# Performance work log

Hardware: AMD Instinct MI355X
Metric: run time of the kernel (lower is better)

Reference implementation:

```python
import jax, jax.numpy as jnp
import numpy as np

S, O, T, C, H = 32, 64, 91, 128, 8  # scenes, objects, timesteps, dim, heads


def setup_inputs() -> dict:
    key = jax.random.key(0)
    ks = jax.random.split(key, 6)
    x = jax.random.normal(ks[0], (S, O, T, C), dtype=jnp.float32)
    valid_mask = jax.random.randint(ks[1], (S, O, T), 0, 2) > 0

    def lin(k, shape):
        return jax.random.normal(k, shape, dtype=jnp.float32) / np.float32(np.sqrt(shape[-1]))

    return dict(
        x=x,
        valid_mask=valid_mask,
        Wqkv_a=lin(ks[2], (3 * C, C)), Wproj_a=lin(ks[3], (C, C)), bproj_a=jnp.zeros((C,), jnp.float32),
        Wqkv_t=lin(ks[4], (3 * C, C)), Wproj_t=lin(ks[5], (C, C)), bproj_t=jnp.zeros((C,), jnp.float32),
    )


def _masked_mha(x, mask, Wqkv, Wproj, bproj):
    # x: (B, N, C); mask: (B, N, N) bool. qkv has no bias, proj has bias.
    B, N, Cd = x.shape
    hd = Cd // H
    scale = hd ** (-0.5)
    qkv = (x @ Wqkv.T).reshape(B, N, 3, H, hd).transpose(2, 0, 3, 1, 4)
    q, k, v = qkv[0], qkv[1], qkv[2]  # (B, H, N, hd)
    s = jnp.einsum('bhnd,bhmd->bhnm', q, k) * scale
    s = jnp.where(mask[:, None], s, -jnp.inf)
    # rows that are fully masked are set to all-zeros (-> uniform softmax), as in torch code
    dead = jnp.all(~mask, axis=-1)  # (B, N)
    s = jnp.where(dead[:, None, :, None], jnp.float32(0.0), s)
    a = jax.nn.softmax(s, axis=-1)
    o = jnp.einsum('bhnm,bhmd->bhnd', a, v).transpose(0, 2, 1, 3).reshape(B, N, Cd)
    return o @ Wproj.T + bproj


def reference(x, valid_mask, Wqkv_a, Wproj_a, bproj_a, Wqkv_t, Wproj_t, bproj_t):
    S_, O_, T_, C_ = x.shape
    # agent-wise attention: attend across objects at each (scene, timestep)
    xa = x.transpose(0, 2, 1, 3).reshape(S_ * T_, O_, C_)
    ma = valid_mask.transpose(0, 2, 1)  # (S, T, O)
    ma = (ma[..., :, None] & ma[..., None, :]).reshape(S_ * T_, O_, O_)
    xa = _masked_mha(xa, ma, Wqkv_a, Wproj_a, bproj_a)
    # time-wise attention: attend across timesteps for each (scene, object)
    xt = xa.reshape(S_, T_, O_, C_).transpose(0, 2, 1, 3).reshape(S_ * O_, T_, C_)
    mt = (valid_mask[..., :, None] & valid_mask[..., None, :]).reshape(S_ * O_, T_, T_)
    xt = _masked_mha(xt, mt, Wqkv_t, Wproj_t, bproj_t)
    return xt.reshape(S_, O_, T_, C_)
```

## Files before the change

### kernel.cpp

```cpp
#include <hip/hip_runtime.h>

#define S_ 32
#define O_ 64
#define T_ 91
#define C_ 128
#define H_ 8

typedef __attribute__((ext_vector_type(8))) short short8;
typedef __attribute__((ext_vector_type(4))) short short4b;
typedef __attribute__((ext_vector_type(4))) float f32x4;

__device__ short g_wqa_h[384 * 128], g_wqa_l[384 * 128];
__device__ short g_wqt_h[384 * 128], g_wqt_l[384 * 128];
__device__ short g_wpa_h[128 * 128], g_wpa_l[128 * 128];
__device__ short g_wpt_h[128 * 128], g_wpt_l[128 * 128];

__device__ __forceinline__ void splitf(float f, short& h, short& l) {
    unsigned u = __float_as_uint(f);
    float hf = __uint_as_float(u & 0xffff0000u);
    h = (short)(u >> 16);
    l = (short)(__float_as_uint(f - hf) >> 16);
}

__device__ __forceinline__ void split8g(const float* p, short8& h, short8& l) {
    float4 a = *(const float4*)p;
    float4 b = *(const float4*)(p + 4);
    float v[8] = {a.x, a.y, a.z, a.w, b.x, b.y, b.z, b.w};
    #pragma unroll
    for (int j = 0; j < 8; ++j) { short hh, ll; splitf(v[j], hh, ll); h[j] = hh; l[j] = ll; }
}

__device__ __forceinline__ void split4v(f32x4 v, short4b& h, short4b& l) {
    #pragma unroll
    for (int j = 0; j < 4; ++j) { short hh, ll; splitf(v[j], hh, ll); h[j] = hh; l[j] = ll; }
}

__global__ __launch_bounds__(256) void prep_all(
    const float* __restrict__ wqa, const float* __restrict__ wqt,
    const float* __restrict__ wpa, const float* __restrict__ wpt)
{
    int t = blockIdx.x * 256 + threadIdx.x;
    const float* src; short* dh; short* dl; int idx;
    if (t < 6144)       { src = wqa; dh = g_wqa_h; dl = g_wqa_l; idx = t; }
    else if (t < 12288) { src = wqt; dh = g_wqt_h; dl = g_wqt_l; idx = t - 6144; }
    else if (t < 14336) { src = wpa; dh = g_wpa_h; dl = g_wpa_l; idx = t - 12288; }
    else                { src = wpt; dh = g_wpt_h; dl = g_wpt_l; idx = t - 14336; }
    int c = idx >> 4, gk = idx & 15;
    int kp = gk >> 2, gg = gk & 3;
    int ct = c >> 4, cl = c & 15;
    const float* s = src + (long)c * C_ + gk * 8;
    long slot = (long)ct * 2048 + kp * 512 + (cl + 16 * gg) * 8;
    short8 vh, vl;
    split8g(s, vh, vl);
    *(short8*)(dh + slot) = vh;
    *(short8*)(dl + slot) = vl;
}

template<int N, int NT, int PASS>
__global__ __launch_bounds__(512) void fused_pass(
    const float* __restrict__ xg, const int* __restrict__ mask,
    const float* __restrict__ bproj, float* __restrict__ yout,
    int bdiv, long bs1, long bs2, long ts, long m1, long m2)
{
    constexpr bool FULL = (NT * 16 == N);
    extern __shared__ char smem[];
    short* xh = (short*)smem;
    short* xl = xh + NT * 2048;
    short* yh = xh;
    short* yl = xl;
    int*   s_m = (int*)(smem + NT * 8192);

    const short* Wh = (PASS == 0) ? g_wqa_h : g_wqt_h;
    const short* Wl = (PASS == 0) ? g_wqa_l : g_wqt_l;
    const short* Ph = (PASS == 0) ? g_wpa_h : g_wpt_h;
    const short* Pl = (PASS == 0) ? g_wpa_l : g_wpt_l;

    const int tid = threadIdx.x;
    const int wv = tid >> 6, l = tid & 63;
    const int ic = l & 15, g = l >> 4;
    const int b = blockIdx.x;
    const int s = b / bdiv, u = b - s * bdiv;
    const long xbase = (long)s * bs1 + (long)u * bs2;
    const long mbase = (long)s * (O_ * T_) + (long)u * m1;

    for (int gi = tid; gi < NT * 256; gi += 512) {
        int token = gi >> 4, cg = gi & 15;
        int kp = cg >> 2, gg = cg & 3;
        int slot = ((token >> 4) * 4 + kp) * 512 + (gg * 16 + (token & 15)) * 8;
        short8 vh, vl;
        if (FULL || token < N) {
            split8g(xg + xbase + (long)token * ts + cg * 8, vh, vl);
        } else {
            #pragma unroll
            for (int j = 0; j < 8; ++j) { vh[j] = 0; vl[j] = 0; }
        }
        *(short8*)(xh + slot) = vh;
        *(short8*)(xl + slot) = vl;
    }
    for (int idx = tid; idx < NT * 16; idx += 512)
        s_m[idx] = (idx < N) ? (mask[mbase + (long)idx * m2] != 0) : 0;
    __syncthreads();

    unsigned jbits = 0, mbits = 0;
    #pragma unroll
    for (int jt = 0; jt < NT; ++jt)
        #pragma unroll
        for (int r = 0; r < 4; ++r) {
            int j = jt * 16 + 4 * g + r;
            if (j < N) {
                jbits |= 1u << (jt * 4 + r);
                if (s_m[j]) mbits |= 1u << (jt * 4 + r);
            }
        }

    const int h = wv;
    f32x4 aQ[NT], aK[NT], aV[NT];
    #pragma unroll
    for (int t2 = 0; t2 < NT; ++t2) {
        aQ[t2] = (f32x4){0.f,0.f,0.f,0.f};
        aK[t2] = (f32x4){0.f,0.f,0.f,0.f};
        aV[t2] = (f32x4){0.f,0.f,0.f,0.f};
    }
    #pragma unroll
    for (int kp = 0; kp < 4; ++kp) {
        short8 wqh = *(const short8*)(Wh + (h * 4 + kp) * 512 + l * 8);
        short8 wql = *(const short8*)(Wl + (h * 4 + kp) * 512 + l * 8);
        short8 wkh = *(const short8*)(Wh + ((8 + h) * 4 + kp) * 512 + l * 8);
        short8 wkl = *(const short8*)(Wl + ((8 + h) * 4 + kp) * 512 + l * 8);
        short8 wvh = *(const short8*)(Wh + ((16 + h) * 4 + kp) * 512 + l * 8);
        short8 wvl = *(const short8*)(Wl + ((16 + h) * 4 + kp) * 512 + l * 8);
        #pragma unroll
        for (int tt = 0; tt < NT; ++tt) {
            short8 xhv = *(const short8*)(xh + (tt * 4 + kp) * 512 + l * 8);
            short8 xlv = *(const short8*)(xl + (tt * 4 + kp) * 512 + l * 8);
            aQ[tt] = __builtin_amdgcn_mfma_f32_16x16x32_bf16(wqh, xhv, aQ[tt], 0, 0, 0);
            aQ[tt] = __builtin_amdgcn_mfma_f32_16x16x32_bf16(wql, xhv, aQ[tt], 0, 0, 0);
            aQ[tt] = __builtin_amdgcn_mfma_f32_16x16x32_bf16(wqh, xlv, aQ[tt], 0, 0, 0);
            aK[tt] = __builtin_amdgcn_mfma_f32_16x16x32_bf16(wkh, xhv, aK[tt], 0, 0, 0);
            aK[tt] = __builtin_amdgcn_mfma_f32_16x16x32_bf16(wkl, xhv, aK[tt], 0, 0, 0);
            aK[tt] = __builtin_amdgcn_mfma_f32_16x16x32_bf16(wkh, xlv, aK[tt], 0, 0, 0);
            aV[tt] = __builtin_amdgcn_mfma_f32_16x16x32_bf16(xhv, wvh, aV[tt], 0, 0, 0);
            aV[tt] = __builtin_amdgcn_mfma_f32_16x16x32_bf16(xlv, wvh, aV[tt], 0, 0, 0);
            aV[tt] = __builtin_amdgcn_mfma_f32_16x16x32_bf16(xhv, wvl, aV[tt], 0, 0, 0);
        }
    }
    const float QS = 0.25f * 1.44269504088896f;
    short4b qfh[NT], qfl[NT], kfh[NT], kfl[NT], vfh[NT], vfl[NT];
    #pragma unroll
    for (int t2 = 0; t2 < NT; ++t2) {
        f32x4 qs = aQ[t2] * QS;
        split4v(qs, qfh[t2], qfl[t2]);
        split4v(aK[t2], kfh[t2], kfl[t2]);
        split4v(aV[t2], vfh[t2], vfl[t2]);
    }
    short8 pwh[4], pwl[4];
    #pragma unroll
    for (int kp = 0; kp < 4; ++kp) {
        pwh[kp] = *(const short8*)(Ph + (wv * 4 + kp) * 512 + l * 8);
        pwl[kp] = *(const short8*)(Pl + (wv * 4 + kp) * 512 + l * 8);
    }
    __syncthreads();

    const int kpw = wv >> 1;
    const int ggw = (2 * wv + (ic >> 3)) & 3;
    const int jw  = ic & 7;

    #pragma unroll
    for (int it = 0; it < NT; ++it) {
        f32x4 sa[NT];
        #pragma unroll
        for (int jt = 0; jt < NT; ++jt) sa[jt] = (f32x4){0.f,0.f,0.f,0.f};
        #pragma unroll
        for (int jt = 0; jt < NT; ++jt) {
            sa[jt] = __builtin_amdgcn_mfma_f32_16x16x16bf16_1k(kfh[jt], qfh[it], sa[jt], 0, 0, 0);
            sa[jt] = __builtin_amdgcn_mfma_f32_16x16x16bf16_1k(kfl[jt], qfh[it], sa[jt], 0, 0, 0);
            sa[jt] = __builtin_amdgcn_mfma_f32_16x16x16bf16_1k(kfh[jt], qfl[it], sa[jt], 0, 0, 0);
        }
        const int query = it * 16 + ic;
        const int qm = s_m[query];
        const unsigned msel = qm ? mbits : jbits;
        float sum = 0.f;
        short4b ph[NT];
        #pragma unroll
        for (int jt = 0; jt < NT; ++jt) {
            #pragma unroll
            for (int r = 0; r < 4; ++r) {
                int bit = (jt << 2) + r;
                float inner = qm ? sa[jt][r] : 0.f;
                float xv = ((msel >> bit) & 1u) ? inner : -1e30f;
                float e = exp2f(xv);
                sum += e;
                unsigned ue = __float_as_uint(e);
                ue += 0x7fffu + ((ue >> 16) & 1u);
                ph[jt][r] = (short)(ue >> 16);
            }
        }
        sum += __shfl_xor(sum, 16, 64);
        sum += __shfl_xor(sum, 32, 64);
        const float inv = 1.f / sum;

        f32x4 pv = (f32x4){0.f,0.f,0.f,0.f};
        #pragma unroll
        for (int kt = 0; kt < NT; ++kt) {
            pv = __builtin_amdgcn_mfma_f32_16x16x16bf16_1k(ph[kt], vfh[kt], pv, 0, 0, 0);
            pv = __builtin_amdgcn_mfma_f32_16x16x16bf16_1k(ph[kt], vfl[kt], pv, 0, 0, 0);
        }
        #pragma unroll
        for (int r = 0; r < 4; ++r) {
            int rloc = 4 * g + r;
            int row = it * 16 + rloc;
            int iv = __builtin_amdgcn_ds_bpermute(rloc << 2, __float_as_int(inv));
            float yv = pv[r] * __int_as_float(iv);
            short hh = 0, ll = 0;
            if (FULL || row < N) splitf(yv, hh, ll);
            int slot = (it * 4 + kpw) * 512 + (ggw * 16 + rloc) * 8 + jw;
            yh[slot] = hh;
            yl[slot] = ll;
        }
    }
    __syncthreads();

    const float bv = bproj[wv * 16 + ic];
    #pragma unroll
    for (int mt = 0; mt < NT; ++mt) {
        f32x4 acc = (f32x4){0.f,0.f,0.f,0.f};
        #pragma unroll
        for (int kp = 0; kp < 4; ++kp) {
            short8 ayh = *(const short8*)(yh + (mt * 4 + kp) * 512 + l * 8);
            short8 ayl = *(const short8*)(yl + (mt * 4 + kp) * 512 + l * 8);
            acc = __builtin_amdgcn_mfma_f32_16x16x32_bf16(ayh, pwh[kp], acc, 0, 0, 0);
            acc = __builtin_amdgcn_mfma_f32_16x16x32_bf16(ayl, pwh[kp], acc, 0, 0, 0);
            acc = __builtin_amdgcn_mfma_f32_16x16x32_bf16(ayh, pwl[kp], acc, 0, 0, 0);
        }
        #pragma unroll
        for (int r = 0; r < 4; ++r) {
            int row = mt * 16 + 4 * g + r;
            if (FULL || row < N)
                yout[((long)b * N + row) * C_ + wv * 16 + ic] = acc[r] + bv;
        }
    }
}

extern "C" void kernel_launch(void* const* d_in, const int* in_sizes, int n_in,
                              void* d_out, int out_size, void* d_ws, size_t ws_size,
                              hipStream_t stream) {
    const float* x       = (const float*)d_in[0];
    const int*   mask    = (const int*)d_in[1];
    const float* Wqkv_a  = (const float*)d_in[2];
    const float* bproj_a = (const float*)d_in[4];
    const float* Wqkv_t  = (const float*)d_in[5];
    const float* bproj_t = (const float*)d_in[7];
    const float* Wproj_a = (const float*)d_in[3];
    const float* Wproj_t = (const float*)d_in[6];
    float* out = (float*)d_out;
    float* xa  = (float*)d_ws;

    prep_all<<<64, 256, 0, stream>>>(Wqkv_a, Wqkv_t, Wproj_a, Wproj_t);

    {
        const size_t lds = 4 * 8192 + 4 * 64;
        fused_pass<O_, 4, 0><<<S_ * T_, 512, lds, stream>>>(
            x, mask, bproj_a, xa,
            T_, (long)O_ * T_ * C_, (long)C_, (long)T_ * C_,
            1L, (long)T_);
    }
    {
        const size_t lds = 6 * 8192 + 6 * 64;
        fused_pass<T_, 6, 1><<<S_ * O_, 512, lds, stream>>>(
            xa, mask, bproj_t, out,
            O_, (long)T_ * O_ * C_, (long)C_, (long)O_ * C_,
            (long)T_, 1L);
    }
}
```

Measured before the change: 313.7 us.

## Cut register pressure to allow two 512-thread blocks per CU

Adds a min-blocks hint to launch bounds, which caps per-thread VGPRs so more blocks can be resident. To make that cap reachable, it splits the QKV projection into a Q/K phase and a separate V phase so fewer accumulators are live at once. It also computes scores one key tile at a time, fused into the softmax loop, and defers loading the projection weights until after attention. It swaps exp2f for the hardware exp2 builtin. If the compiler cannot fit the cap, spills may appear, and splitting V out re-reads the x tiles from LDS.

Result: slower. 851.5 us (+171.4%).

```diff
diff --git a/kernel.cpp b/kernel.cpp
--- a/kernel.cpp
+++ b/kernel.cpp
@@ -57,7 +57,7 @@
 }
 
 template<int N, int NT, int PASS>
-__global__ __launch_bounds__(512) void fused_pass(
+__global__ __launch_bounds__(512, 4) void fused_pass(
     const float* __restrict__ xg, const int* __restrict__ mask,
     const float* __restrict__ bproj, float* __restrict__ yout,
     int bdiv, long bs1, long bs2, long ts, long m1, long m2)
@@ -114,50 +114,60 @@
         }
 
     const int h = wv;
-    f32x4 aQ[NT], aK[NT], aV[NT];
-    #pragma unroll
-    for (int t2 = 0; t2 < NT; ++t2) {
-        aQ[t2] = (f32x4){0.f,0.f,0.f,0.f};
-        aK[t2] = (f32x4){0.f,0.f,0.f,0.f};
-        aV[t2] = (f32x4){0.f,0.f,0.f,0.f};
-    }
-    #pragma unroll
-    for (int kp = 0; kp < 4; ++kp) {
-        short8 wqh = *(const short8*)(Wh + (h * 4 + kp) * 512 + l * 8);
-        short8 wql = *(const short8*)(Wl + (h * 4 + kp) * 512 + l * 8);
-        short8 wkh = *(const short8*)(Wh + ((8 + h) * 4 + kp) * 512 + l * 8);
-        short8 wkl = *(const short8*)(Wl + ((8 + h) * 4 + kp) * 512 + l * 8);
-        short8 wvh = *(const short8*)(Wh + ((16 + h) * 4 + kp) * 512 + l * 8);
-        short8 wvl = *(const short8*)(Wl + ((16 + h) * 4 + kp) * 512 + l * 8);
-        #pragma unroll
-        for (int tt = 0; tt < NT; ++tt) {
-            short8 xhv = *(const short8*)(xh + (tt * 4 + kp) * 512 + l * 8);
-            short8 xlv = *(const short8*)(xl + (tt * 4 + kp) * 512 + l * 8);
-            aQ[tt] = __builtin_amdgcn_mfma_f32_16x16x32_bf16(wqh, xhv, aQ[tt], 0, 0, 0);
-            aQ[tt] = __builtin_amdgcn_mfma_f32_16x16x32_bf16(wql, xhv, aQ[tt], 0, 0, 0);
-            aQ[tt] = __builtin_amdgcn_mfma_f32_16x16x32_bf16(wqh, xlv, aQ[tt], 0, 0, 0);
-            aK[tt] = __builtin_amdgcn_mfma_f32_16x16x32_bf16(wkh, xhv, aK[tt], 0, 0, 0);
-            aK[tt] = __builtin_amdgcn_mfma_f32_16x16x32_bf16(wkl, xhv, aK[tt], 0, 0, 0);
-            aK[tt] = __builtin_amdgcn_mfma_f32_16x16x32_bf16(wkh, xlv, aK[tt], 0, 0, 0);
-            aV[tt] = __builtin_amdgcn_mfma_f32_16x16x32_bf16(xhv, wvh, aV[tt], 0, 0, 0);
-            aV[tt] = __builtin_amdgcn_mfma_f32_16x16x32_bf16(xlv, wvh, aV[tt], 0, 0, 0);
-            aV[tt] = __builtin_amdgcn_mfma_f32_16x16x32_bf16(xhv, wvl, aV[tt], 0, 0, 0);
-        }
-    }
     const float QS = 0.25f * 1.44269504088896f;
-    short4b qfh[NT], qfl[NT], kfh[NT], kfl[NT], vfh[NT], vfl[NT];
-    #pragma unroll
-    for (int t2 = 0; t2 < NT; ++t2) {
-        f32x4 qs = aQ[t2] * QS;
-        split4v(qs, qfh[t2], qfl[t2]);
-        split4v(aK[t2], kfh[t2], kfl[t2]);
-        split4v(aV[t2], vfh[t2], vfl[t2]);
-    }
-    short8 pwh[4], pwl[4];
-    #pragma unroll
-    for (int kp = 0; kp < 4; ++kp) {
-        pwh[kp] = *(const short8*)(Ph + (wv * 4 + kp) * 512 + l * 8);
-        pwl[kp] = *(const short8*)(Pl + (wv * 4 + kp) * 512 + l * 8);
+    short4b qfh[NT], qfl[NT], kfh[NT], kfl[NT];
+    {
+        f32x4 aQ[NT], aK[NT];
+        #pragma unroll
+        for (int t2 = 0; t2 < NT; ++t2) {
+            aQ[t2] = (f32x4){0.f,0.f,0.f,0.f};
+            aK[t2] = (f32x4){0.f,0.f,0.f,0.f};
+        }
+        #pragma unroll
+        for (int kp = 0; kp < 4; ++kp) {
+            short8 wqh = *(const short8*)(Wh + (h * 4 + kp) * 512 + l * 8);
+            short8 wql = *(const short8*)(Wl + (h * 4 + kp) * 512 + l * 8);
+            short8 wkh = *(const short8*)(Wh + ((8 + h) * 4 + kp) * 512 + l * 8);
+            short8 wkl = *(const short8*)(Wl + ((8 + h) * 4 + kp) * 512 + l * 8);
+            #pragma unroll
+            for (int tt = 0; tt < NT; ++tt) {
+                short8 xhv = *(const short8*)(xh + (tt * 4 + kp) * 512 + l * 8);
+                short8 xlv = *(const short8*)(xl + (tt * 4 + kp) * 512 + l * 8);
+                aQ[tt] = __builtin_amdgcn_mfma_f32_16x16x32_bf16(wqh, xhv, aQ[tt], 0, 0, 0);
+                aQ[tt] = __builtin_amdgcn_mfma_f32_16x16x32_bf16(wql, xhv, aQ[tt], 0, 0, 0);
+                aQ[tt] = __builtin_amdgcn_mfma_f32_16x16x32_bf16(wqh, xlv, aQ[tt], 0, 0, 0);
+                aK[tt] = __builtin_amdgcn_mfma_f32_16x16x32_bf16(wkh, xhv, aK[tt], 0, 0, 0);
+                aK[tt] = __builtin_amdgcn_mfma_f32_16x16x32_bf16(wkl, xhv, aK[tt], 0, 0, 0);
+                aK[tt] = __builtin_amdgcn_mfma_f32_16x16x32_bf16(wkh, xlv, aK[tt], 0, 0, 0);
+            }
+        }
+        #pragma unroll
+        for (int t2 = 0; t2 < NT; ++t2) {
+            f32x4 qs = aQ[t2] * QS;
+            split4v(qs, qfh[t2], qfl[t2]);
+            split4v(aK[t2], kfh[t2], kfl[t2]);
+        }
+    }
+    short4b vfh[NT], vfl[NT];
+    {
+        f32x4 aV[NT];
+        #pragma unroll
+        for (int t2 = 0; t2 < NT; ++t2) aV[t2] = (f32x4){0.f,0.f,0.f,0.f};
+        #pragma unroll
+        for (int kp = 0; kp < 4; ++kp) {
+            short8 wvh = *(const short8*)(Wh + ((16 + h) * 4 + kp) * 512 + l * 8);
+            short8 wvl = *(const short8*)(Wl + ((16 + h) * 4 + kp) * 512 + l * 8);
+            #pragma unroll
+            for (int tt = 0; tt < NT; ++tt) {
+                short8 xhv = *(const short8*)(xh + (tt * 4 + kp) * 512 + l * 8);
+                short8 xlv = *(const short8*)(xl + (tt * 4 + kp) * 512 + l * 8);
+                aV[tt] = __builtin_amdgcn_mfma_f32_16x16x32_bf16(xhv, wvh, aV[tt], 0, 0, 0);
+                aV[tt] = __builtin_amdgcn_mfma_f32_16x16x32_bf16(xlv, wvh, aV[tt], 0, 0, 0);
+                aV[tt] = __builtin_amdgcn_mfma_f32_16x16x32_bf16(xhv, wvl, aV[tt], 0, 0, 0);
+            }
+        }
+        #pragma unroll
+        for (int t2 = 0; t2 < NT; ++t2) split4v(aV[t2], vfh[t2], vfl[t2]);
     }
     __syncthreads();
 
@@ -167,15 +177,6 @@
 
     #pragma unroll
     for (int it = 0; it < NT; ++it) {
-        f32x4 sa[NT];
-        #pragma unroll
-        for (int jt = 0; jt < NT; ++jt) sa[jt] = (f32x4){0.f,0.f,0.f,0.f};
-        #pragma unroll
-        for (int jt = 0; jt < NT; ++jt) {
-            sa[jt] = __builtin_amdgcn_mfma_f32_16x16x16bf16_1k(kfh[jt], qfh[it], sa[jt], 0, 0, 0);
-            sa[jt] = __builtin_amdgcn_mfma_f32_16x16x16bf16_1k(kfl[jt], qfh[it], sa[jt], 0, 0, 0);
-            sa[jt] = __builtin_amdgcn_mfma_f32_16x16x16bf16_1k(kfh[jt], qfl[it], sa[jt], 0, 0, 0);
-        }
         const int query = it * 16 + ic;
         const int qm = s_m[query];
         const unsigned msel = qm ? mbits : jbits;
@@ -183,12 +184,16 @@
         short4b ph[NT];
         #pragma unroll
         for (int jt = 0; jt < NT; ++jt) {
+            f32x4 sa = (f32x4){0.f,0.f,0.f,0.f};
+            sa = __builtin_amdgcn_mfma_f32_16x16x16bf16_1k(kfh[jt], qfh[it], sa, 0, 0, 0);
+            sa = __builtin_amdgcn_mfma_f32_16x16x16bf16_1k(kfl[jt], qfh[it], sa, 0, 0, 0);
+            sa = __builtin_amdgcn_mfma_f32_16x16x16bf16_1k(kfh[jt], qfl[it], sa, 0, 0, 0);
             #pragma unroll
             for (int r = 0; r < 4; ++r) {
                 int bit = (jt << 2) + r;
-                float inner = qm ? sa[jt][r] : 0.f;
+                float inner = qm ? sa[r] : 0.f;
                 float xv = ((msel >> bit) & 1u) ? inner : -1e30f;
-                float e = exp2f(xv);
+                float e = __builtin_amdgcn_exp2f(xv);
                 sum += e;
                 unsigned ue = __float_as_uint(e);
                 ue += 0x7fffu + ((ue >> 16) & 1u);
@@ -220,6 +225,12 @@
     }
     __syncthreads();
 
+    short8 pwh[4], pwl[4];
+    #pragma unroll
+    for (int kp = 0; kp < 4; ++kp) {
+        pwh[kp] = *(const short8*)(Ph + (wv * 4 + kp) * 512 + l * 8);
+        pwl[kp] = *(const short8*)(Pl + (wv * 4 + kp) * 512 + l * 8);
+    }
     const float bv = bproj[wv * 16 + ic];
     #pragma unroll
     for (int mt = 0; mt < NT; ++mt) {
@@ -247,11 +258,11 @@
     const float* x       = (const float*)d_in[0];
     const int*   mask    = (const int*)d_in[1];
     const float* Wqkv_a  = (const float*)d_in[2];
+    const float* Wproj_a = (const float*)d_in[3];
     const float* bproj_a = (const float*)d_in[4];
     const float* Wqkv_t  = (const float*)d_in[5];
+    const float* Wproj_t = (const float*)d_in[6];
     const float* bproj_t = (const float*)d_in[7];
-    const float* Wproj_a = (const float*)d_in[3];
-    const float* Wproj_t = (const float*)d_in[6];
     float* out = (float*)d_out;
     float* xa  = (float*)d_ws;
 
```
